# Optimization experiments

Hardware: AMD Instinct MI355X
Metric: run time of the kernel (lower is better)

The kernel has to match this reference:

```python
import jax, jax.numpy as jnp
import numpy as np

C_CONST = 8.0   # RG-LRU decay constant (Griffin/Hawk)
EPS = 1e-6      # RMSNorm eps
K = 4           # causal depthwise conv kernel size


def rmsnorm(x, w):
    # x: [B,S,D]
    var = jnp.mean(x * x, axis=-1, keepdims=True)
    return x * jax.lax.rsqrt(var + EPS) * w


def causal_depthwise_conv(x, conv_w, conv_b):
    # x: [B,S,D], conv_w: [K,D], conv_b: [D]; causal (left-pad K-1)
    B, S, D = x.shape
    xp = jnp.pad(x, ((0, 0), (K - 1, 0), (0, 0)))
    out = conv_b
    for k in range(K):  # tiny fixed loop over kernel taps
        out = out + conv_w[k] * xp[:, k:k + S, :]
    return out


def rg_lru(x, Wi, Wa, lam):
    # x: [B,S,D]; diagonal linear recurrence h_t = a_t*h_{t-1} + sqrt(1-a_t^2)*(i_t*x_t)
    r = jax.nn.sigmoid(jnp.einsum('bsd,de->bse', x, Wa))   # recurrence gate
    i = jax.nn.sigmoid(jnp.einsum('bsd,de->bse', x, Wi))   # input gate
    log_a = -C_CONST * jax.nn.softplus(lam) * r            # [B,S,D]
    a = jnp.exp(log_a)
    b = jnp.sqrt(jnp.maximum(1.0 - a * a, 1e-12)) * (i * x)

    def comb(e1, e2):
        a1, b1 = e1
        a2, b2 = e2
        return (a1 * a2, a2 * b1 + b2)

    _, h = jax.lax.associative_scan(comb, (a, b), axis=1)
    return h


def setup_inputs() -> dict:
    key = jax.random.key(0)
    ks = jax.random.split(key, 16)
    B, S, D, H = 4, 2048, 1024, 4096
    s = 0.02
    return {
        'x': jax.random.normal(ks[0], (B, S, D), jnp.float32),
        'norm1_w': jnp.ones((D,), jnp.float32),
        'Wx': jax.random.normal(ks[1], (D, D), jnp.float32) * s,
        'Wy': jax.random.normal(ks[2], (D, D), jnp.float32) * s,
        'conv_w': jax.random.normal(ks[3], (K, D), jnp.float32) * s,
        'conv_b': jnp.zeros((D,), jnp.float32),
        'Wi': jax.random.normal(ks[4], (D, D), jnp.float32) * s,
        'Wa': jax.random.normal(ks[5], (D, D), jnp.float32) * s,
        'lam': jax.random.normal(ks[6], (D,), jnp.float32) * 0.5,
        'Wo': jax.random.normal(ks[7], (D, D), jnp.float32) * s,
        'norm2_w': jnp.ones((D,), jnp.float32),
        'Wg': jax.random.normal(ks[8], (D, H), jnp.float32) * s,
        'Wu': jax.random.normal(ks[9], (D, H), jnp.float32) * s,
        'Wd': jax.random.normal(ks[10], (H, D), jnp.float32) * s,
    }


def reference(x, norm1_w, Wx, Wy, conv_w, conv_b, Wi, Wa, lam, Wo,
              norm2_w, Wg, Wu, Wd):
    # --- mixing block (Hawk recurrent block) with pre-norm + residual ---
    t = rmsnorm(x, norm1_w)
    xb = jnp.einsum('bsd,de->bse', t, Wx)          # recurrence branch
    xb = causal_depthwise_conv(xb, conv_w, conv_b)
    h = rg_lru(xb, Wi, Wa, lam)
    yb = jax.nn.gelu(jnp.einsum('bsd,de->bse', t, Wy))  # gate branch
    mix = jnp.einsum('bsd,de->bse', h * yb, Wo)
    h1 = x + mix
    # --- gated MLP with pre-norm + residual ---
    u = rmsnorm(h1, norm2_w)
    ffn = jnp.einsum('bsh,hd->bsd', jax.nn.gelu(jnp.einsum('bsd,dh->bsh', u, Wg)) * jnp.einsum('bsd,dh->bsh', u, Wu), Wd)
    return h1 + ffn
```

## Files before the change

### kernel.cpp

```cpp
#include <hip/hip_runtime.h>
#include <hip/hip_bf16.h>
#include <stdint.h>

#define B_SZ   4
#define S_LEN  2048
#define D_DIM  1024
#define H_DIM  4096
#define T_TOK  (B_SZ * S_LEN)
#define NC     32
#define CL     64

typedef unsigned short u16;
typedef unsigned int   u32;
typedef __attribute__((ext_vector_type(8))) short short8;
typedef __attribute__((ext_vector_type(4))) float f32x4;

__device__ __forceinline__ float tof(u16 u) {
    union { u32 i; float f; } v; v.i = ((u32)u) << 16; return v.f;
}
__device__ __forceinline__ u16 tobf(float f) {
    union { float f; u32 i; } v; v.f = f;
    u32 x = v.i;
    return (u16)((x + 0x7FFFu + ((x >> 16) & 1u)) >> 16);
}

__device__ __forceinline__ float gelu_f(float x) {
    float x3 = x * x * x;
    float tin = 0.7978845608028654f * (x + 0.044715f * x3);
    float e = __expf(2.f * tin);
    float th = 1.f - 2.f / (e + 1.f);
    return 0.5f * x * (1.f + th);
}
__device__ __forceinline__ float sig_f(float x) {
    return 1.f / (1.f + __expf(-x));
}

__device__ __forceinline__ void gload16(const void* g, void* l) {
    __builtin_amdgcn_global_load_lds(
        (const __attribute__((address_space(1))) u32*)g,
        (__attribute__((address_space(3))) u32*)l,
        16, 0, 0);
}

__global__ void detect_k(const u32* __restrict__ w, int* __restrict__ flag) {
    if (blockIdx.x == 0 && threadIdx.x == 0)
        *flag = (w[0] == 0x3F800000u) ? 1 : 0;
}

__global__ __launch_bounds__(256) void convert_k(
    const void* __restrict__ src, u16* __restrict__ dst, int n,
    const int* __restrict__ flag) {
    int i = blockIdx.x * 256 + threadIdx.x;
    if (i < n) {
        if (*flag) dst[i] = tobf(((const float*)src)[i]);
        else       dst[i] = ((const u16*)src)[i];
    }
}

__global__ __launch_bounds__(256) void transpose_any(
    const void* __restrict__ W, u16* __restrict__ WT, int R, int C,
    const int* __restrict__ flag) {
    __shared__ u16 tile[32][33];
    bool f32 = (*flag) != 0;
    int tx = threadIdx.x & 31, ty = threadIdx.x >> 5;
    int c0 = blockIdx.x * 32, r0 = blockIdx.y * 32;
#pragma unroll
    for (int k = 0; k < 4; k++) {
        size_t idx = (size_t)(r0 + ty + k * 8) * C + c0 + tx;
        tile[ty + k * 8][tx] = f32 ? tobf(((const float*)W)[idx])
                                   : ((const u16*)W)[idx];
    }
    __syncthreads();
#pragma unroll
    for (int k = 0; k < 4; k++)
        WT[(size_t)(c0 + ty + k * 8) * R + r0 + tx] = tile[tx][ty + k * 8];
}

__global__ __launch_bounds__(256) void rmsnorm_any(
    const void* __restrict__ X, const u16* __restrict__ Wt, u16* __restrict__ O,
    const int* __restrict__ flagp, int in_mode) {
    bool f32 = in_mode == 1 || (*flagp != 0);
    int row = blockIdx.x;
    int t = threadIdx.x;
    float x0, x1, x2, x3;
    if (f32) {
        float4 v = ((const float4*)((const float*)X + (size_t)row * D_DIM))[t];
        x0 = v.x; x1 = v.y; x2 = v.z; x3 = v.w;
    } else {
        uint2 pv = ((const uint2*)((const u16*)X + (size_t)row * D_DIM))[t];
        x0 = tof(pv.x & 0xffff); x1 = tof(pv.x >> 16);
        x2 = tof(pv.y & 0xffff); x3 = tof(pv.y >> 16);
    }
    float ss = x0 * x0 + x1 * x1 + x2 * x2 + x3 * x3;
#pragma unroll
    for (int off = 32; off; off >>= 1) ss += __shfl_down(ss, off, 64);
    __shared__ float red[4];
    if ((t & 63) == 0) red[t >> 6] = ss;
    __syncthreads();
    float tot = red[0] + red[1] + red[2] + red[3];
    float rs = rsqrtf(tot * (1.f / D_DIM) + 1e-6f);
    uint2 wv = ((const uint2*)Wt)[t];
    float w0 = tof(wv.x & 0xffff), w1 = tof(wv.x >> 16);
    float w2 = tof(wv.y & 0xffff), w3 = tof(wv.y >> 16);
    uint2 ov;
    ov.x = (u32)tobf(x0 * rs * w0) | ((u32)tobf(x1 * rs * w1) << 16);
    ov.y = (u32)tobf(x2 * rs * w2) | ((u32)tobf(x3 * rs * w3) << 16);
    ((uint2*)(O + (size_t)row * D_DIM))[t] = ov;
}

__global__ __launch_bounds__(256) void conv_k(
    const u16* __restrict__ xb, const u16* __restrict__ cw,
    const u16* __restrict__ cb, u16* __restrict__ xc) {
    size_t idx2 = (size_t)blockIdx.x * 256 + threadIdx.x;
    int dp = (int)(idx2 % (D_DIM / 2));
    size_t ts = idx2 / (D_DIM / 2);
    int s = (int)(ts % S_LEN);
    int d0 = dp * 2;
    float a0 = tof(cb[d0]), a1 = tof(cb[d0 + 1]);
    long long base = (long long)ts * D_DIM + d0;
#pragma unroll
    for (int k = 0; k < 4; k++) {
        int sp = s + k - 3;
        if (sp >= 0) {
            long long off = base + (long long)(k - 3) * D_DIM;
            a0 += tof(cw[k * D_DIM + d0]) * tof(xb[off]);
            a1 += tof(cw[k * D_DIM + d0 + 1]) * tof(xb[off + 1]);
        }
    }
    xc[base] = tobf(a0);
    xc[base + 1] = tobf(a1);
}

__global__ void acoef_any(const void* __restrict__ lam, float* __restrict__ acoef,
                          const int* __restrict__ flagp) {
    int d = blockIdx.x * 256 + threadIdx.x;
    if (d < D_DIM) {
        float l = (*flagp) ? ((const float*)lam)[d] : tof(((const u16*)lam)[d]);
        float sp = fmaxf(l, 0.f) + log1pf(__expf(-fabsf(l)));
        acoef[d] = -8.f * sp;
    }
}

__global__ __launch_bounds__(256) void gates_chunk_k(
    const u16* __restrict__ r, const u16* __restrict__ ii, const u16* __restrict__ xc,
    const float* __restrict__ acoef, float* __restrict__ Ap, float* __restrict__ Bs) {
    int d = blockIdx.x * 256 + threadIdx.x;
    int c = blockIdx.y, b = blockIdx.z;
    float ac = acoef[d];
    size_t base = ((size_t)(b * S_LEN) + c * CL) * D_DIM + d;
    float ap = 1.f, bs = 0.f;
    for (int tt = 0; tt < CL; tt++) {
        float rv = tof(r[base]), iv = tof(ii[base]), xv = tof(xc[base]);
        float a = __expf(ac * rv);
        float bv = sqrtf(fmaxf(1.f - a * a, 1e-12f)) * (iv * xv);
        ap *= a;
        bs = fmaf(a, bs, bv);
        base += D_DIM;
    }
    size_t o = ((size_t)(b * NC) + c) * D_DIM + d;
    Ap[o] = ap; Bs[o] = bs;
}

__global__ __launch_bounds__(256) void carry_k(
    const float* __restrict__ Ap, const float* __restrict__ Bs, float* __restrict__ carry) {
    int d = blockIdx.x * 256 + threadIdx.x;
    int b = blockIdx.y;
    float h = 0.f;
    for (int c = 0; c < NC; c++) {
        size_t o = ((size_t)(b * NC) + c) * D_DIM + d;
        carry[o] = h;
        h = fmaf(Ap[o], h, Bs[o]);
    }
}

__global__ __launch_bounds__(256) void apply_k(
    const u16* __restrict__ r, const u16* __restrict__ ii, const u16* __restrict__ xc,
    const float* __restrict__ acoef, const float* __restrict__ carry,
    const u16* __restrict__ yb, u16* __restrict__ g) {
    int d = blockIdx.x * 256 + threadIdx.x;
    int c = blockIdx.y, b = blockIdx.z;
    float ac = acoef[d];
    float h = carry[((size_t)(b * NC) + c) * D_DIM + d];
    size_t base = ((size_t)(b * S_LEN) + c * CL) * D_DIM + d;
    for (int tt = 0; tt < CL; tt++) {
        float rv = tof(r[base]), iv = tof(ii[base]), xv = tof(xc[base]);
        float a = __expf(ac * rv);
        float bv = sqrtf(fmaxf(1.f - a * a, 1e-12f)) * (iv * xv);
        h = fmaf(a, h, bv);
        g[base] = tobf(h * tof(yb[base]));
        base += D_DIM;
    }
}

#define BM 128
#define BN 128
#define BK 32

enum { EPI_NONE = 0, EPI_GELU = 1, EPI_SIG = 2, EPI_RESID = 3, EPI_MUL = 4 };

template <int EPI, bool OUTF32>
__global__ __launch_bounds__(256) void gemm_bt(
    const u16* __restrict__ A, const u16* __restrict__ BT,
    void* __restrict__ Cv, const void* __restrict__ aux,
    const int* __restrict__ flagp, int aux_mode,
    int M, int N, int K) {
    __shared__ __align__(16) u16 As[BM * BK];
    __shared__ __align__(16) u16 Bs[BN * BK];
    const int t = threadIdx.x;
    const int lane = t & 63;
    const int w = t >> 6;
    const int wm = w >> 1, wn = w & 1;
    const int quad = lane >> 4, l16 = lane & 15;

    const int m0 = blockIdx.y * BM;
    const int n0 = blockIdx.x * BN;

    const int srow = t >> 2;
    const int scol = (t & 3) * 16;
    const char* ag  = (const char*)A  + ((size_t)(m0 + srow) * K) * 2 + scol;
    const char* ag2 = ag + (size_t)64 * K * 2;
    const char* bg  = (const char*)BT + ((size_t)(n0 + srow) * K) * 2 + scol;
    const char* bg2 = bg + (size_t)64 * K * 2;
    char* lA  = (char*)As + t * 16;
    char* lA2 = lA + 4096;
    char* lB  = (char*)Bs + t * 16;
    char* lB2 = lB + 4096;

    f32x4 acc[4][4];
#pragma unroll
    for (int i = 0; i < 4; i++)
#pragma unroll
        for (int j = 0; j < 4; j++) acc[i][j] = (f32x4){0.f, 0.f, 0.f, 0.f};

    for (int k0 = 0; k0 < K; k0 += BK) {
        __syncthreads();
        gload16(ag, lA);
        gload16(ag2, lA2);
        gload16(bg, lB);
        gload16(bg2, lB2);
        ag += 64; ag2 += 64; bg += 64; bg2 += 64;
        __syncthreads();

        short8 af[4], bf[4];
#pragma unroll
        for (int i = 0; i < 4; i++) {
            int row = wm * 64 + i * 16 + l16;
            af[i] = *(const short8*)&As[row * 32 + quad * 8];
        }
#pragma unroll
        for (int j = 0; j < 4; j++) {
            int row = wn * 64 + j * 16 + l16;
            bf[j] = *(const short8*)&Bs[row * 32 + quad * 8];
        }
#pragma unroll
        for (int i = 0; i < 4; i++)
#pragma unroll
            for (int j = 0; j < 4; j++)
                acc[i][j] = __builtin_amdgcn_mfma_f32_16x16x32_bf16(
                    af[i], bf[j], acc[i][j], 0, 0, 0);
    }

    bool auxF32 = (aux_mode == 2) || (aux_mode == 1 && *flagp != 0);

#pragma unroll
    for (int i = 0; i < 4; i++) {
        int mbase = m0 + wm * 64 + i * 16 + quad * 4;
#pragma unroll
        for (int j = 0; j < 4; j++) {
            int n = n0 + wn * 64 + j * 16 + l16;
#pragma unroll
            for (int rr = 0; rr < 4; rr++) {
                size_t idx = (size_t)(mbase + rr) * N + n;
                float v = acc[i][j][rr];
                if (EPI == EPI_GELU) v = gelu_f(v);
                else if (EPI == EPI_SIG) v = sig_f(v);
                else if (EPI == EPI_RESID) {
                    float avv = auxF32 ? ((const float*)aux)[idx]
                                       : tof(((const u16*)aux)[idx]);
                    v = v + avv;
                } else if (EPI == EPI_MUL) {
                    float avv = auxF32 ? ((const float*)aux)[idx]
                                       : tof(((const u16*)aux)[idx]);
                    v = v * avv;
                }
                if (OUTF32) ((float*)Cv)[idx] = v;
                else        ((u16*)Cv)[idx] = tobf(v);
            }
        }
    }
}

extern "C" void kernel_launch(void* const* d_in, const int* in_sizes, int n_in,
                              void* d_out, int out_size, void* d_ws, size_t ws_size,
                              hipStream_t stream) {
    const void* x      = d_in[0];
    const void* n1w    = d_in[1];
    const void* Wx     = d_in[2];
    const void* Wy     = d_in[3];
    const void* conv_w = d_in[4];
    const void* conv_b = d_in[5];
    const void* Wi     = d_in[6];
    const void* Wa     = d_in[7];
    const void* lam    = d_in[8];
    const void* Wo     = d_in[9];
    const void* n2w    = d_in[10];
    const void* Wg     = d_in[11];
    const void* Wu     = d_in[12];
    const void* Wd     = d_in[13];
    float* out = (float*)d_out;

    char* ws = (char*)d_ws;
    auto alloc = [&](size_t bytes) {
        char* p = ws;
        ws += (bytes + 255) & ~(size_t)255;
        return p;
    };
    const size_t DH = (size_t)D_DIM * H_DIM * 2;
    const size_t TD = (size_t)T_TOK * D_DIM * 2;
    const size_t TH = (size_t)T_TOK * H_DIM * 2;

    int*  dflag  = (int*)alloc(256);
    u16*  n1wc   = (u16*)alloc(D_DIM * 2);
    u16*  n2wc   = (u16*)alloc(D_DIM * 2);
    u16*  cwc    = (u16*)alloc(4 * D_DIM * 2);
    u16*  cbc    = (u16*)alloc(D_DIM * 2);
    float* acoef = (float*)alloc(D_DIM * 4);
    float* Ap    = (float*)alloc((size_t)B_SZ * NC * D_DIM * 4);
    float* Bsm   = (float*)alloc((size_t)B_SZ * NC * D_DIM * 4);
    float* carry = (float*)alloc((size_t)B_SZ * NC * D_DIM * 4);
    u16* WT      = (u16*)alloc(DH);
    u16* T0 = (u16*)alloc(TD);
    u16* T1 = (u16*)alloc(TD);
    u16* T2 = (u16*)alloc(TD);
    u16* T3 = (u16*)alloc(TD);
    u16* T4 = (u16*)alloc(TD);
    u16* ggb = (u16*)alloc(TH);
    float* h1f = (float*)alloc((size_t)T_TOK * D_DIM * 4);

    dim3 b256(256);

    detect_k<<<dim3(1), dim3(64), 0, stream>>>((const u32*)n1w, dflag);
    convert_k<<<dim3(4), b256, 0, stream>>>(n1w, n1wc, D_DIM, dflag);
    convert_k<<<dim3(4), b256, 0, stream>>>(n2w, n2wc, D_DIM, dflag);
    convert_k<<<dim3(16), b256, 0, stream>>>(conv_w, cwc, 4 * D_DIM, dflag);
    convert_k<<<dim3(4), b256, 0, stream>>>(conv_b, cbc, D_DIM, dflag);
    acoef_any<<<dim3(4), b256, 0, stream>>>(lam, acoef, dflag);

    rmsnorm_any<<<dim3(T_TOK), b256, 0, stream>>>(x, n1wc, T2, dflag, 0);

    transpose_any<<<dim3(32, 32), b256, 0, stream>>>(Wx, WT, D_DIM, D_DIM, dflag);
    gemm_bt<EPI_NONE, false><<<dim3(D_DIM / BN, T_TOK / BM), b256, 0, stream>>>(
        T2, WT, T1, nullptr, dflag, 0, T_TOK, D_DIM, D_DIM);

    transpose_any<<<dim3(32, 32), b256, 0, stream>>>(Wy, WT, D_DIM, D_DIM, dflag);
    gemm_bt<EPI_GELU, false><<<dim3(D_DIM / BN, T_TOK / BM), b256, 0, stream>>>(
        T2, WT, T3, nullptr, dflag, 0, T_TOK, D_DIM, D_DIM);

    conv_k<<<dim3((T_TOK * D_DIM / 2) / 256), b256, 0, stream>>>(T1, cwc, cbc, T0);

    transpose_any<<<dim3(32, 32), b256, 0, stream>>>(Wa, WT, D_DIM, D_DIM, dflag);
    gemm_bt<EPI_SIG, false><<<dim3(D_DIM / BN, T_TOK / BM), b256, 0, stream>>>(
        T0, WT, T4, nullptr, dflag, 0, T_TOK, D_DIM, D_DIM);
    transpose_any<<<dim3(32, 32), b256, 0, stream>>>(Wi, WT, D_DIM, D_DIM, dflag);
    gemm_bt<EPI_SIG, false><<<dim3(D_DIM / BN, T_TOK / BM), b256, 0, stream>>>(
        T0, WT, T2, nullptr, dflag, 0, T_TOK, D_DIM, D_DIM);

    gates_chunk_k<<<dim3(D_DIM / 256, NC, B_SZ), b256, 0, stream>>>(T4, T2, T0, acoef, Ap, Bsm);
    carry_k<<<dim3(D_DIM / 256, B_SZ), b256, 0, stream>>>(Ap, Bsm, carry);
    apply_k<<<dim3(D_DIM / 256, NC, B_SZ), b256, 0, stream>>>(T4, T2, T0, acoef, carry, T3, T4);

    transpose_any<<<dim3(32, 32), b256, 0, stream>>>(Wo, WT, D_DIM, D_DIM, dflag);
    gemm_bt<EPI_RESID, true><<<dim3(D_DIM / BN, T_TOK / BM), b256, 0, stream>>>(
        T4, WT, h1f, x, dflag, 1, T_TOK, D_DIM, D_DIM);

    rmsnorm_any<<<dim3(T_TOK), b256, 0, stream>>>(h1f, n2wc, T1, dflag, 1);

    transpose_any<<<dim3(128, 32), b256, 0, stream>>>(Wg, WT, D_DIM, H_DIM, dflag);
    gemm_bt<EPI_GELU, false><<<dim3(H_DIM / BN, T_TOK / BM), b256, 0, stream>>>(
        T1, WT, ggb, nullptr, dflag, 0, T_TOK, H_DIM, D_DIM);
    transpose_any<<<dim3(128, 32), b256, 0, stream>>>(Wu, WT, D_DIM, H_DIM, dflag);
    gemm_bt<EPI_MUL, false><<<dim3(H_DIM / BN, T_TOK / BM), b256, 0, stream>>>(
        T1, WT, ggb, ggb, dflag, 0, T_TOK, H_DIM, D_DIM);

    transpose_any<<<dim3(32, 128), b256, 0, stream>>>(Wd, WT, H_DIM, D_DIM, dflag);
    gemm_bt<EPI_RESID, true><<<dim3(D_DIM / BN, T_TOK / BM), b256, 0, stream>>>(
        ggb, WT, out, h1f, dflag, 2, T_TOK, D_DIM, H_DIM);
}
```

Before: 810.0 us.

## Fuse paired projection GEMMs, widen BK, vectorize conv and scan kernels

Pairs of GEMMs that share an input (Wx/Wy and Wa/Wi) now run as one launch over concatenated transposed weights, and each half of the output gets its own epilogue. GEMM BK grows from 32 to 64, which halves the number of K-loop barriers. The Wd GEMM gets a block-index swizzle to improve L2 reuse. The conv and scan kernels are vectorized (8 and 2 elements per thread), and the scan now uses 64 chunks of length 32. Small parameter-prep kernels are merged into one launch. Risks are extra LDS use, which may lower occupancy, and a different traffic pattern for the chunked scan.

```diff
diff --git a/kernel.cpp b/kernel.cpp
--- a/kernel.cpp
+++ b/kernel.cpp
@@ -7,8 +7,8 @@
 #define D_DIM  1024
 #define H_DIM  4096
 #define T_TOK  (B_SZ * S_LEN)
-#define NC     32
-#define CL     64
+#define NC     64
+#define CL     32
 
 typedef unsigned short u16;
 typedef unsigned int   u32;
@@ -22,6 +22,12 @@
     union { float f; u32 i; } v; v.f = f;
     u32 x = v.i;
     return (u16)((x + 0x7FFFu + ((x >> 16) & 1u)) >> 16);
+}
+__device__ __forceinline__ void unp8(uint4 v, float* f) {
+    f[0] = tof(v.x & 0xffff); f[1] = tof(v.x >> 16);
+    f[2] = tof(v.y & 0xffff); f[3] = tof(v.y >> 16);
+    f[4] = tof(v.z & 0xffff); f[5] = tof(v.z >> 16);
+    f[6] = tof(v.w & 0xffff); f[7] = tof(v.w >> 16);
 }
 
 __device__ __forceinline__ float gelu_f(float x) {
@@ -47,13 +53,24 @@
         *flag = (w[0] == 0x3F800000u) ? 1 : 0;
 }
 
-__global__ __launch_bounds__(256) void convert_k(
-    const void* __restrict__ src, u16* __restrict__ dst, int n,
-    const int* __restrict__ flag) {
+__global__ __launch_bounds__(256) void prep_small(
+    const void* n1w, const void* n2w, const void* cw, const void* cb,
+    const void* lam, u16* n1wc, u16* n2wc, u16* cwc, u16* cbc,
+    float* acoef, const int* __restrict__ flagp) {
     int i = blockIdx.x * 256 + threadIdx.x;
-    if (i < n) {
-        if (*flag) dst[i] = tobf(((const float*)src)[i]);
-        else       dst[i] = ((const u16*)src)[i];
+    bool f32 = (*flagp) != 0;
+    auto rd = [&](const void* p, int j) {
+        return f32 ? ((const float*)p)[j] : tof(((const u16*)p)[j]);
+    };
+    if (i < 1024) n1wc[i] = tobf(rd(n1w, i));
+    else if (i < 2048) n2wc[i - 1024] = tobf(rd(n2w, i - 1024));
+    else if (i < 6144) cwc[i - 2048] = tobf(rd(cw, i - 2048));
+    else if (i < 7168) cbc[i - 6144] = tobf(rd(cb, i - 6144));
+    else {
+        int d = i - 7168;
+        float l = rd(lam, d);
+        float sp = fmaxf(l, 0.f) + log1pf(__expf(-fabsf(l)));
+        acoef[d] = -8.f * sp;
     }
 }
 
@@ -111,99 +128,130 @@
 __global__ __launch_bounds__(256) void conv_k(
     const u16* __restrict__ xb, const u16* __restrict__ cw,
     const u16* __restrict__ cb, u16* __restrict__ xc) {
-    size_t idx2 = (size_t)blockIdx.x * 256 + threadIdx.x;
-    int dp = (int)(idx2 % (D_DIM / 2));
-    size_t ts = idx2 / (D_DIM / 2);
-    int s = (int)(ts % S_LEN);
-    int d0 = dp * 2;
-    float a0 = tof(cb[d0]), a1 = tof(cb[d0 + 1]);
-    long long base = (long long)ts * D_DIM + d0;
+    size_t idx = (size_t)blockIdx.x * 256 + threadIdx.x;
+    int dp = (int)(idx & 127);
+    size_t ts = idx >> 7;
+    int s = (int)(ts & (S_LEN - 1));
+    int d0 = dp * 8;
+    float acc[8];
+    unp8(*(const uint4*)(cb + d0), acc);
+    size_t base = ts * D_DIM + d0;
 #pragma unroll
     for (int k = 0; k < 4; k++) {
         int sp = s + k - 3;
         if (sp >= 0) {
-            long long off = base + (long long)(k - 3) * D_DIM;
-            a0 += tof(cw[k * D_DIM + d0]) * tof(xb[off]);
-            a1 += tof(cw[k * D_DIM + d0 + 1]) * tof(xb[off + 1]);
+            float xf[8], wf[8];
+            unp8(*(const uint4*)(xb + base + (ptrdiff_t)(k - 3) * D_DIM), xf);
+            unp8(*(const uint4*)(cw + k * D_DIM + d0), wf);
+#pragma unroll
+            for (int e = 0; e < 8; e++) acc[e] += wf[e] * xf[e];
         }
     }
-    xc[base] = tobf(a0);
-    xc[base + 1] = tobf(a1);
-}
-
-__global__ void acoef_any(const void* __restrict__ lam, float* __restrict__ acoef,
-                          const int* __restrict__ flagp) {
-    int d = blockIdx.x * 256 + threadIdx.x;
-    if (d < D_DIM) {
-        float l = (*flagp) ? ((const float*)lam)[d] : tof(((const u16*)lam)[d]);
-        float sp = fmaxf(l, 0.f) + log1pf(__expf(-fabsf(l)));
-        acoef[d] = -8.f * sp;
-    }
+    uint4 ov;
+    ov.x = (u32)tobf(acc[0]) | ((u32)tobf(acc[1]) << 16);
+    ov.y = (u32)tobf(acc[2]) | ((u32)tobf(acc[3]) << 16);
+    ov.z = (u32)tobf(acc[4]) | ((u32)tobf(acc[5]) << 16);
+    ov.w = (u32)tobf(acc[6]) | ((u32)tobf(acc[7]) << 16);
+    *(uint4*)(xc + base) = ov;
 }
 
 __global__ __launch_bounds__(256) void gates_chunk_k(
     const u16* __restrict__ r, const u16* __restrict__ ii, const u16* __restrict__ xc,
-    const float* __restrict__ acoef, float* __restrict__ Ap, float* __restrict__ Bs) {
-    int d = blockIdx.x * 256 + threadIdx.x;
+    const float* __restrict__ acoef, float2* __restrict__ Ap2, float2* __restrict__ Bs2) {
+    int d2 = blockIdx.x * 256 + threadIdx.x;
     int c = blockIdx.y, b = blockIdx.z;
-    float ac = acoef[d];
-    size_t base = ((size_t)(b * S_LEN) + c * CL) * D_DIM + d;
-    float ap = 1.f, bs = 0.f;
+    float ac0 = acoef[d2 * 2], ac1 = acoef[d2 * 2 + 1];
+    const u32* r2 = (const u32*)r;
+    const u32* i2 = (const u32*)ii;
+    const u32* x2 = (const u32*)xc;
+    size_t base = ((size_t)b * S_LEN + c * CL) * (D_DIM / 2) + d2;
+    float ap0 = 1.f, bs0 = 0.f, ap1 = 1.f, bs1 = 0.f;
     for (int tt = 0; tt < CL; tt++) {
-        float rv = tof(r[base]), iv = tof(ii[base]), xv = tof(xc[base]);
-        float a = __expf(ac * rv);
-        float bv = sqrtf(fmaxf(1.f - a * a, 1e-12f)) * (iv * xv);
-        ap *= a;
-        bs = fmaf(a, bs, bv);
-        base += D_DIM;
-    }
-    size_t o = ((size_t)(b * NC) + c) * D_DIM + d;
-    Ap[o] = ap; Bs[o] = bs;
+        u32 rv = r2[base], iv = i2[base], xv = x2[base];
+        float a0 = __expf(ac0 * tof(rv & 0xffff));
+        float a1 = __expf(ac1 * tof(rv >> 16));
+        float b0 = sqrtf(fmaxf(1.f - a0 * a0, 1e-12f)) * (tof(iv & 0xffff) * tof(xv & 0xffff));
+        float b1 = sqrtf(fmaxf(1.f - a1 * a1, 1e-12f)) * (tof(iv >> 16) * tof(xv >> 16));
+        ap0 *= a0; bs0 = fmaf(a0, bs0, b0);
+        ap1 *= a1; bs1 = fmaf(a1, bs1, b1);
+        base += D_DIM / 2;
+    }
+    size_t o = ((size_t)b * NC + c) * (D_DIM / 2) + d2;
+    Ap2[o] = make_float2(ap0, ap1);
+    Bs2[o] = make_float2(bs0, bs1);
 }
 
 __global__ __launch_bounds__(256) void carry_k(
-    const float* __restrict__ Ap, const float* __restrict__ Bs, float* __restrict__ carry) {
-    int d = blockIdx.x * 256 + threadIdx.x;
+    const float2* __restrict__ Ap2, const float2* __restrict__ Bs2,
+    float2* __restrict__ carry2) {
+    int d2 = blockIdx.x * 256 + threadIdx.x;
     int b = blockIdx.y;
-    float h = 0.f;
+    float2 h = make_float2(0.f, 0.f);
     for (int c = 0; c < NC; c++) {
-        size_t o = ((size_t)(b * NC) + c) * D_DIM + d;
-        carry[o] = h;
-        h = fmaf(Ap[o], h, Bs[o]);
+        size_t o = ((size_t)b * NC + c) * (D_DIM / 2) + d2;
+        float2 ap = Ap2[o], bs = Bs2[o];
+        carry2[o] = h;
+        h.x = fmaf(ap.x, h.x, bs.x);
+        h.y = fmaf(ap.y, h.y, bs.y);
     }
 }
 
 __global__ __launch_bounds__(256) void apply_k(
     const u16* __restrict__ r, const u16* __restrict__ ii, const u16* __restrict__ xc,
-    const float* __restrict__ acoef, const float* __restrict__ carry,
+    const float* __restrict__ acoef, const float2* __restrict__ carry2,
     const u16* __restrict__ yb, u16* __restrict__ g) {
-    int d = blockIdx.x * 256 + threadIdx.x;
+    int d2 = blockIdx.x * 256 + threadIdx.x;
     int c = blockIdx.y, b = blockIdx.z;
-    float ac = acoef[d];
-    float h = carry[((size_t)(b * NC) + c) * D_DIM + d];
-    size_t base = ((size_t)(b * S_LEN) + c * CL) * D_DIM + d;
+    float ac0 = acoef[d2 * 2], ac1 = acoef[d2 * 2 + 1];
+    float2 h = carry2[((size_t)b * NC + c) * (D_DIM / 2) + d2];
+    const u32* r2 = (const u32*)r;
+    const u32* i2 = (const u32*)ii;
+    const u32* x2 = (const u32*)xc;
+    const u32* y2 = (const u32*)yb;
+    u32* g2 = (u32*)g;
+    size_t base = ((size_t)b * S_LEN + c * CL) * (D_DIM / 2) + d2;
     for (int tt = 0; tt < CL; tt++) {
-        float rv = tof(r[base]), iv = tof(ii[base]), xv = tof(xc[base]);
-        float a = __expf(ac * rv);
-        float bv = sqrtf(fmaxf(1.f - a * a, 1e-12f)) * (iv * xv);
-        h = fmaf(a, h, bv);
-        g[base] = tobf(h * tof(yb[base]));
-        base += D_DIM;
+        u32 rv = r2[base], iv = i2[base], xv = x2[base], yv = y2[base];
+        float a0 = __expf(ac0 * tof(rv & 0xffff));
+        float a1 = __expf(ac1 * tof(rv >> 16));
+        float b0 = sqrtf(fmaxf(1.f - a0 * a0, 1e-12f)) * (tof(iv & 0xffff) * tof(xv & 0xffff));
+        float b1 = sqrtf(fmaxf(1.f - a1 * a1, 1e-12f)) * (tof(iv >> 16) * tof(xv >> 16));
+        h.x = fmaf(a0, h.x, b0);
+        h.y = fmaf(a1, h.y, b1);
+        g2[base] = (u32)tobf(h.x * tof(yv & 0xffff)) |
+                   ((u32)tobf(h.y * tof(yv >> 16)) << 16);
+        base += D_DIM / 2;
     }
 }
 
 #define BM 128
 #define BN 128
-#define BK 32
+#define BK 64
 
 enum { EPI_NONE = 0, EPI_GELU = 1, EPI_SIG = 2, EPI_RESID = 3, EPI_MUL = 4 };
 
-template <int EPI, bool OUTF32>
+template <int E>
+__device__ __forceinline__ float epi_apply(float v, const void* aux, size_t idx,
+                                           bool auxF32) {
+    if (E == EPI_GELU) return gelu_f(v);
+    if (E == EPI_SIG) return sig_f(v);
+    if (E == EPI_RESID) {
+        float a = auxF32 ? ((const float*)aux)[idx] : tof(((const u16*)aux)[idx]);
+        return v + a;
+    }
+    if (E == EPI_MUL) {
+        float a = auxF32 ? ((const float*)aux)[idx] : tof(((const u16*)aux)[idx]);
+        return v * a;
+    }
+    return v;
+}
+
+template <int EPI0, int EPI1, bool OUTF32, bool SWZ>
 __global__ __launch_bounds__(256) void gemm_bt(
     const u16* __restrict__ A, const u16* __restrict__ BT,
-    void* __restrict__ Cv, const void* __restrict__ aux,
+    void* __restrict__ C0v, void* __restrict__ C1v, const void* __restrict__ aux,
     const int* __restrict__ flagp, int aux_mode,
-    int M, int N, int K) {
+    int M, int N, int K, int halfN) {
     __shared__ __align__(16) u16 As[BM * BK];
     __shared__ __align__(16) u16 Bs[BN * BK];
     const int t = threadIdx.x;
@@ -212,19 +260,26 @@
     const int wm = w >> 1, wn = w & 1;
     const int quad = lane >> 4, l16 = lane & 15;
 
-    const int m0 = blockIdx.y * BM;
-    const int n0 = blockIdx.x * BN;
-
-    const int srow = t >> 2;
-    const int scol = (t & 3) * 16;
-    const char* ag  = (const char*)A  + ((size_t)(m0 + srow) * K) * 2 + scol;
-    const char* ag2 = ag + (size_t)64 * K * 2;
-    const char* bg  = (const char*)BT + ((size_t)(n0 + srow) * K) * 2 + scol;
-    const char* bg2 = bg + (size_t)64 * K * 2;
-    char* lA  = (char*)As + t * 16;
-    char* lA2 = lA + 4096;
-    char* lB  = (char*)Bs + t * 16;
-    char* lB2 = lB + 4096;
+    int mt, nt;
+    if (SWZ) {
+        int GN = gridDim.x;
+        int L = blockIdx.y * GN + blockIdx.x;
+        int per = (GN * gridDim.y) >> 3;
+        int id = (L & 7) * per + (L >> 3);
+        mt = id / GN; nt = id - mt * GN;
+    } else {
+        mt = blockIdx.y; nt = blockIdx.x;
+    }
+    const int m0 = mt * BM;
+    const int n0 = nt * BN;
+
+    const int srow = t >> 3;
+    const int scol = (t & 7) * 16;
+    const char* ag = (const char*)A + ((size_t)(m0 + srow) * K) * 2 + scol;
+    const char* bg = (const char*)BT + ((size_t)(n0 + srow) * K) * 2 + scol;
+    char* lA = (char*)As + srow * 128 + scol;
+    char* lB = (char*)Bs + srow * 128 + scol;
+    const size_t rstep = (size_t)32 * K * 2;
 
     f32x4 acc[4][4];
 #pragma unroll
@@ -234,55 +289,52 @@
 
     for (int k0 = 0; k0 < K; k0 += BK) {
         __syncthreads();
-        gload16(ag, lA);
-        gload16(ag2, lA2);
-        gload16(bg, lB);
-        gload16(bg2, lB2);
-        ag += 64; ag2 += 64; bg += 64; bg2 += 64;
+#pragma unroll
+        for (int rr = 0; rr < 4; rr++) {
+            gload16(ag + rr * rstep, lA + rr * 32 * 128);
+            gload16(bg + rr * rstep, lB + rr * 32 * 128);
+        }
+        ag += 128; bg += 128;
         __syncthreads();
 
-        short8 af[4], bf[4];
-#pragma unroll
-        for (int i = 0; i < 4; i++) {
-            int row = wm * 64 + i * 16 + l16;
-            af[i] = *(const short8*)&As[row * 32 + quad * 8];
+#pragma unroll
+        for (int kk = 0; kk < 2; kk++) {
+            short8 af[4], bf[4];
+#pragma unroll
+            for (int i = 0; i < 4; i++) {
+                int row = wm * 64 + i * 16 + l16;
+                af[i] = *(const short8*)&As[row * 64 + kk * 32 + quad * 8];
+            }
+#pragma unroll
+            for (int j = 0; j < 4; j++) {
+                int row = wn * 64 + j * 16 + l16;
+                bf[j] = *(const short8*)&Bs[row * 64 + kk * 32 + quad * 8];
+            }
+#pragma unroll
+            for (int i = 0; i < 4; i++)
+#pragma unroll
+                for (int j = 0; j < 4; j++)
+                    acc[i][j] = __builtin_amdgcn_mfma_f32_16x16x32_bf16(
+                        af[i], bf[j], acc[i][j], 0, 0, 0);
         }
-#pragma unroll
-        for (int j = 0; j < 4; j++) {
-            int row = wn * 64 + j * 16 + l16;
-            bf[j] = *(const short8*)&Bs[row * 32 + quad * 8];
-        }
-#pragma unroll
-        for (int i = 0; i < 4; i++)
-#pragma unroll
-            for (int j = 0; j < 4; j++)
-                acc[i][j] = __builtin_amdgcn_mfma_f32_16x16x32_bf16(
-                    af[i], bf[j], acc[i][j], 0, 0, 0);
-    }
-
-    bool auxF32 = (aux_mode == 2) || (aux_mode == 1 && *flagp != 0);
+    }
+
+    const bool auxF32 = (aux_mode == 2) || (aux_mode == 1 && *flagp != 0);
+    const int side = (n0 >= halfN) ? 1 : 0;
+    void* Cv = side ? C1v : C0v;
 
 #pragma unroll
     for (int i = 0; i < 4; i++) {
         int mbase = m0 + wm * 64 + i * 16 + quad * 4;
 #pragma unroll
         for (int j = 0; j < 4; j++) {
-            int n = n0 + wn * 64 + j * 16 + l16;
+            int ncol = n0 - side * halfN + wn * 64 + j * 16 + l16;
 #pragma unroll
             for (int rr = 0; rr < 4; rr++) {
-                size_t idx = (size_t)(mbase + rr) * N + n;
+                size_t idx = (size_t)(mbase + rr) * halfN + ncol;
                 float v = acc[i][j][rr];
-                if (EPI == EPI_GELU) v = gelu_f(v);
-                else if (EPI == EPI_SIG) v = sig_f(v);
-                else if (EPI == EPI_RESID) {
-                    float avv = auxF32 ? ((const float*)aux)[idx]
-                                       : tof(((const u16*)aux)[idx]);
-                    v = v + avv;
-                } else if (EPI == EPI_MUL) {
-                    float avv = auxF32 ? ((const float*)aux)[idx]
-                                       : tof(((const u16*)aux)[idx]);
-                    v = v * avv;
-                }
+                v = side ? epi_apply<EPI1>(v, aux, idx, auxF32)
+                         : epi_apply<EPI0>(v, aux, idx, auxF32);
                 if (OUTF32) ((float*)Cv)[idx] = v;
                 else        ((u16*)Cv)[idx] = tobf(v);
             }
@@ -315,6 +367,7 @@
         ws += (bytes + 255) & ~(size_t)255;
         return p;
     };
+    const size_t DD = (size_t)D_DIM * D_DIM;
     const size_t DH = (size_t)D_DIM * H_DIM * 2;
     const size_t TD = (size_t)T_TOK * D_DIM * 2;
     const size_t TH = (size_t)T_TOK * H_DIM * 2;
@@ -325,64 +378,62 @@
     u16*  cwc    = (u16*)alloc(4 * D_DIM * 2);
     u16*  cbc    = (u16*)alloc(D_DIM * 2);
     float* acoef = (float*)alloc(D_DIM * 4);
-    float* Ap    = (float*)alloc((size_t)B_SZ * NC * D_DIM * 4);
-    float* Bsm   = (float*)alloc((size_t)B_SZ * NC * D_DIM * 4);
-    float* carry = (float*)alloc((size_t)B_SZ * NC * D_DIM * 4);
-    u16* WT      = (u16*)alloc(DH);
-    u16* T0 = (u16*)alloc(TD);
-    u16* T1 = (u16*)alloc(TD);
-    u16* T2 = (u16*)alloc(TD);
-    u16* T3 = (u16*)alloc(TD);
-    u16* T4 = (u16*)alloc(TD);
+    float2* Ap2    = (float2*)alloc((size_t)B_SZ * NC * D_DIM * 4);
+    float2* Bs2    = (float2*)alloc((size_t)B_SZ * NC * D_DIM * 4);
+    float2* carry2 = (float2*)alloc((size_t)B_SZ * NC * D_DIM * 4);
+    u16* WT  = (u16*)alloc(DH);
+    u16* T0  = (u16*)alloc(TD);
+    u16* T1  = (u16*)alloc(TD);
+    u16* T2  = (u16*)alloc(TD);
+    u16* T3  = (u16*)alloc(TD);
+    u16* T4  = (u16*)alloc(TD);
     u16* ggb = (u16*)alloc(TH);
     float* h1f = (float*)alloc((size_t)T_TOK * D_DIM * 4);
 
     dim3 b256(256);
 
     detect_k<<<dim3(1), dim3(64), 0, stream>>>((const u32*)n1w, dflag);
-    convert_k<<<dim3(4), b256, 0, stream>>>(n1w, n1wc, D_DIM, dflag);
-    convert_k<<<dim3(4), b256, 0, stream>>>(n2w, n2wc, D_DIM, dflag);
-    convert_k<<<dim3(16), b256, 0, stream>>>(conv_w, cwc, 4 * D_DIM, dflag);
-    convert_k<<<dim3(4), b256, 0, stream>>>(conv_b, cbc, D_DIM, dflag);
-    acoef_any<<<dim3(4), b256, 0, stream>>>(lam, acoef, dflag);
+    prep_small<<<dim3(32), b256, 0, stream>>>(n1w, n2w, conv_w, conv_b, lam,
+                                              n1wc, n2wc, cwc, cbc, acoef, dflag);
 
     rmsnorm_any<<<dim3(T_TOK), b256, 0, stream>>>(x, n1wc, T2, dflag, 0);
 
     transpose_any<<<dim3(32, 32), b256, 0, stream>>>(Wx, WT, D_DIM, D_DIM, dflag);
-    gemm_bt<EPI_NONE, false><<<dim3(D_DIM / BN, T_TOK / BM), b256, 0, stream>>>(
-        T2, WT, T1, nullptr, dflag, 0, T_TOK, D_DIM, D_DIM);
-
-    transpose_any<<<dim3(32, 32), b256, 0, stream>>>(Wy, WT, D_DIM, D_DIM, dflag);
-    gemm_bt<EPI_GELU, false><<<dim3(D_DIM / BN, T_TOK / BM), b256, 0, stream>>>(
-        T2, WT, T3, nullptr, dflag, 0, T_TOK, D_DIM, D_DIM);
-
-    conv_k<<<dim3((T_TOK * D_DIM / 2) / 256), b256, 0, stream>>>(T1, cwc, cbc, T0);
+    transpose_any<<<dim3(32, 32), b256, 0, stream>>>(Wy, WT + DD, D_DIM, D_DIM, dflag);
+    gemm_bt<EPI_NONE, EPI_GELU, false, false>
+        <<<dim3(2 * D_DIM / BN, T_TOK / BM), b256, 0, stream>>>(
+        T2, WT, T1, T3, nullptr, dflag, 0, T_TOK, 2 * D_DIM, D_DIM, D_DIM);
+
+    conv_k<<<dim3(T_TOK * D_DIM / 8 / 256), b256, 0, stream>>>(T1, cwc, cbc, T0);
 
     transpose_any<<<dim3(32, 32), b256, 0, stream>>>(Wa, WT, D_DIM, D_DIM, dflag);
-    gemm_bt<EPI_SIG, false><<<dim3(D_DIM / BN, T_TOK / BM), b256, 0, stream>>>(
-        T0, WT, T4, nullptr, dflag, 0, T_TOK, D_DIM, D_DIM);
-    transpose_any<<<dim3(32, 32), b256, 0, stream>>>(Wi, WT, D_DIM, D_DIM, dflag);
-    gemm_bt<EPI_SIG, false><<<dim3(D_DIM / BN, T_TOK / BM), b256, 0, stream>>>(
-        T0, WT, T2, nullptr, dflag, 0, T_TOK, D_DIM, D_DIM);
-
-    gates_chunk_k<<<dim3(D_DIM / 256, NC, B_SZ), b256, 0, stream>>>(T4, T2, T0, acoef, Ap, Bsm);
-    carry_k<<<dim3(D_DIM / 256, B_SZ), b256, 0, stream>>>(Ap, Bsm, carry);
-    apply_k<<<dim3(D_DIM / 256, NC, B_SZ), b256, 0, stream>>>(T4, T2, T0, acoef, carry, T3, T4);
+    transpose_any<<<dim3(32, 32), b256, 0, stream>>>(Wi, WT + DD, D_DIM, D_DIM, dflag);
+    gemm_bt<EPI_SIG, EPI_SIG, false, false>
+        <<<dim3(2 * D_DIM / BN, T_TOK / BM), b256, 0, stream>>>(
+        T0, WT, T4, T2, nullptr, dflag, 0, T_TOK, 2 * D_DIM, D_DIM, D_DIM);
+
+    gates_chunk_k<<<dim3(2, NC, B_SZ), b256, 0, stream>>>(T4, T2, T0, acoef, Ap2, Bs2);
+    carry_k<<<dim3(2, B_SZ), b256, 0, stream>>>(Ap2, Bs2, carry2);
+    apply_k<<<dim3(2, NC, B_SZ), b256, 0, stream>>>(T4, T2, T0, acoef, carry2, T3, T4);
 
     transpose_any<<<dim3(32, 32), b256, 0, stream>>>(Wo, WT, D_DIM, D_DIM, dflag);
-    gemm_bt<EPI_RESID, true><<<dim3(D_DIM / BN, T_TOK / BM), b256, 0, stream>>>(
-        T4, WT, h1f, x, dflag, 1, T_TOK, D_DIM, D_DIM);
+    gemm_bt<EPI_RESID, EPI_RESID, true, false>
+        <<<dim3(D_DIM / BN, T_TOK / BM), b256, 0, stream>>>(
+        T4, WT, h1f, h1f, x, dflag, 1, T_TOK, D_DIM, D_DIM, D_DIM);
 
     rmsnorm_any<<<dim3(T_TOK), b256, 0, stream>>>(h1f, n2wc, T1, dflag, 1);
 
     transpose_any<<<dim3(128, 32), b256, 0, stream>>>(Wg, WT, D_DIM, H_DIM, dflag);
-    gemm_bt<EPI_GELU, false><<<dim3(H_DIM / BN, T_TOK / BM), b256, 0, stream>>>(
-        T1, WT, ggb, nullptr, dflag, 0, T_TOK, H_DIM, D_DIM);
+    gemm_bt<EPI_GELU, EPI_GELU, false, false>
+        <<<dim3(H_DIM / BN, T_TOK / BM), b256, 0, stream>>>(
+        T1, WT, ggb, ggb, nullptr, dflag, 0, T_TOK, H_DIM, D_DIM, H_DIM);
     transpose_any<<<dim3(128, 32), b256, 0, stream>>>(Wu, WT, D_DIM, H_DIM, dflag);
-    gemm_bt<EPI_MUL, false><<<dim3(H_DIM / BN, T_TOK / BM), b256, 0, stream>>>(
-        T1, WT, ggb, ggb, dflag, 0, T_TOK, H_DIM, D_DIM);
+    gemm_bt<EPI_MUL, EPI_MUL, false, false>
+        <<<dim3(H_DIM / BN, T_TOK / BM), b256, 0, stream>>>(
+        T1, WT, ggb, ggb, ggb, dflag, 0, T_TOK, H_DIM, D_DIM, H_DIM);
 
     transpose_any<<<dim3(32, 128), b256, 0, stream>>>(Wd, WT, H_DIM, D_DIM, dflag);
-    gemm_bt<EPI_RESID, true><<<dim3(D_DIM / BN, T_TOK / BM), b256, 0, stream>>>(
-        ggb, WT, out, h1f, dflag, 2, T_TOK, D_DIM, H_DIM);
-}
+    gemm_bt<EPI_RESID, EPI_RESID, true, true>
+        <<<dim3(D_DIM / BN, T_TOK / BM), b256, 0, stream>>>(
+        ggb, WT, out, out, h1f, dflag, 2, T_TOK, D_DIM, H_DIM, D_DIM);
+}
```

Result: no change. 826.0 us (+2.0%).
